# Kernel tuning notes

Hardware: AMD Instinct MI355X
Metric: run time of the kernel (lower is better)

Reference implementation:

```python
import jax, jax.numpy as jnp
import numpy as np

QMAX = 127.0  # int8 symmetric fake-quant (Brevitas weight_bit_width=8)

def fake_quant_w(w):
    # per-tensor symmetric int8 fake quantization of weights
    scale = jnp.maximum(jnp.max(jnp.abs(w)), 1e-8) / QMAX
    return jnp.clip(jnp.round(w / scale), -QMAX, QMAX) * scale

def conv2d(x, w, b=None, padding=0, groups=1):
    y = jax.lax.conv_general_dilated(
        x, w, window_strides=(1, 1),
        padding=[(padding, padding), (padding, padding)],
        feature_group_count=groups,
        dimension_numbers=('NCHW', 'OIHW', 'NCHW'))
    if b is not None:
        y = y + b[None, :, None, None]
    return y

def setup_inputs() -> dict:
    key = jax.random.key(0)
    ks = jax.random.split(key, 12)
    B, H, W = 16, 96, 128
    cor_planes = 4 * (2 * 3 + 1) ** 2  # 196
    def rnd(k, shape, fan_in):
        return jax.random.normal(k, shape, dtype=jnp.float32) * (1.0 / np.sqrt(fan_in))
    return {
        'flow': jax.random.normal(ks[0], (B, 2, H, W), dtype=jnp.float32),
        'corr': jax.random.normal(ks[1], (B, cor_planes, H, W), dtype=jnp.float32),
        'Wc1': rnd(ks[2], (96, cor_planes, 1, 1), cor_planes),
        'bc1': rnd(ks[3], (96,), cor_planes),
        'Wf1': rnd(ks[4], (64, 2, 1, 1), 2),
        'bf1': rnd(ks[5], (64,), 2),
        'Wf2': rnd(ks[6], (32, 64, 1, 1), 64),
        'bf2': rnd(ks[7], (32,), 64),
        'Wd': rnd(ks[8], (128, 1, 3, 3), 9),   # depthwise, groups=128, no bias
        'Wp': rnd(ks[9], (80, 128, 1, 1), 128),
        'bp': rnd(ks[10], (80,), 128),
    }

def reference(flow, corr, Wc1, bc1, Wf1, bf1, Wf2, bf2, Wd, Wp, bp):
    relu = jax.nn.relu
    cor = relu(conv2d(corr, fake_quant_w(Wc1), bc1))              # [B,96,H,W]
    flo = relu(conv2d(flow, fake_quant_w(Wf1), bf1))              # [B,64,H,W]
    flo = relu(conv2d(flo, fake_quant_w(Wf2), bf2))               # [B,32,H,W]
    cor_flo = jnp.concatenate([cor, flo], axis=1)                 # [B,128,H,W]
    dw = conv2d(cor_flo, fake_quant_w(Wd), None, padding=1, groups=128)  # depthwise 3x3
    out = relu(conv2d(dw, fake_quant_w(Wp), bp))                  # [B,80,H,W]
    return jnp.concatenate([out, flow], axis=1)                   # [B,82,H,W]
```

## Files before the change

kernel.cpp:

```cpp
#include <hip/hip_runtime.h>

typedef unsigned short ushort_t;
typedef __attribute__((ext_vector_type(8))) short short8;
typedef __attribute__((ext_vector_type(4))) float f32x4;

#define HWp 12288
#define NB  16

#define OFF_WFRAG1 0
#define OFF_WFRAG2 43008
#define OFF_WF1T   63488
#define OFF_WF2T   64000
#define OFF_WDQ    72192
#define OFF_CORFLO 131072

__device__ __forceinline__ short f2bf(float f) {
  unsigned u = __builtin_bit_cast(unsigned, f);
  u = (u + 0x7FFFu + ((u >> 16) & 1u)) >> 16;
  return (short)u;
}
__device__ __forceinline__ float bf2f(ushort_t u) {
  return __builtin_bit_cast(float, (unsigned)u << 16);
}
__device__ __forceinline__ int swz(int a16) { return a16 ^ ((a16 >> 2) & 3); }

__global__ __launch_bounds__(1024) void quant_pack(
    const float* __restrict__ Wc1, const float* __restrict__ Wf1,
    const float* __restrict__ Wf2, const float* __restrict__ Wd,
    const float* __restrict__ Wp, char* __restrict__ ws)
{
  int t = blockIdx.x;
  const float* src; int n;
  if      (t == 0) { src = Wc1; n = 96*196; }
  else if (t == 1) { src = Wf1; n = 128; }
  else if (t == 2) { src = Wf2; n = 2048; }
  else if (t == 3) { src = Wd;  n = 1152; }
  else             { src = Wp;  n = 10240; }

  __shared__ float red[1024];
  float m = 0.f;
  for (int i = threadIdx.x; i < n; i += 1024) m = fmaxf(m, fabsf(src[i]));
  red[threadIdx.x] = m;
  __syncthreads();
  for (int s = 512; s > 0; s >>= 1) {
    if (threadIdx.x < s) red[threadIdx.x] = fmaxf(red[threadIdx.x], red[threadIdx.x + s]);
    __syncthreads();
  }
  float scale = fmaxf(red[0], 1e-8f) / 127.0f;

  if (t == 0) {
    short* dst = (short*)(ws + OFF_WFRAG1);
    for (int i = threadIdx.x; i < 21504; i += 1024) {
      int j = i & 7, lane = (i >> 3) & 63, rest = i >> 9;
      int mb = rest % 6, kb = rest / 6;
      int ch = mb*16 + (lane & 15);
      int k  = kb*32 + ((lane >> 4) << 3) + j;
      float v = 0.f;
      if (k < 196) {
        float q = rintf(src[ch*196 + k] / scale);
        v = fminf(fmaxf(q, -127.f), 127.f) * scale;
      }
      dst[i] = f2bf(v);
    }
  } else if (t == 4) {
    short* dst = (short*)(ws + OFF_WFRAG2);
    for (int i = threadIdx.x; i < 10240; i += 1024) {
      int j = i & 7, lane = (i >> 3) & 63, rest = i >> 9;
      int mb = rest % 5, kb = rest / 5;
      int ch = mb*16 + (lane & 15);
      int k  = kb*32 + ((lane >> 4) << 3) + j;
      float q = rintf(src[ch*128 + k] / scale);
      dst[i] = f2bf(fminf(fmaxf(q, -127.f), 127.f) * scale);
    }
  } else if (t == 1) {
    float* dst = (float*)(ws + OFF_WF1T);
    for (int i = threadIdx.x; i < 128; i += 1024) {
      int o = i >> 1, c = i & 1;
      float q = rintf(src[i] / scale);
      dst[c*64 + o] = fminf(fmaxf(q, -127.f), 127.f) * scale;
    }
  } else if (t == 2) {
    float* dst = (float*)(ws + OFF_WF2T);
    for (int i = threadIdx.x; i < 2048; i += 1024) {
      int o = i >> 6, c = i & 63;
      float q = rintf(src[i] / scale);
      dst[c*32 + o] = fminf(fmaxf(q, -127.f), 127.f) * scale;
    }
  } else {
    float* dst = (float*)(ws + OFF_WDQ);
    for (int i = threadIdx.x; i < 1152; i += 1024) {
      float q = rintf(src[i] / scale);
      dst[i] = fminf(fmaxf(q, -127.f), 127.f) * scale;
    }
  }
}

__global__ __launch_bounds__(256, 4) void stage1_mfma(
    const float* __restrict__ corr, const float* __restrict__ bc1,
    char* __restrict__ ws)
{
  __shared__ ushort_t s_act[28*64*8];
  const int t = threadIdx.x;
  const int b = blockIdx.x / 192;
  const int pix_base = (blockIdx.x % 192) * 64;

  for (int i = t; i < 1792; i += 256) {
    int px = i & 63, kg = i >> 6, k0 = kg << 3;
    const float* src = corr + ((size_t)b*196 + k0)*HWp + pix_base + px;
    short8 v;
    if (kg < 24) {
#pragma unroll
      for (int j = 0; j < 8; j++) v[j] = f2bf(src[(size_t)j*HWp]);
    } else if (kg == 24) {
#pragma unroll
      for (int j = 0; j < 8; j++) v[j] = (j < 4) ? f2bf(src[(size_t)j*HWp]) : (short)0;
    } else {
#pragma unroll
      for (int j = 0; j < 8; j++) v[j] = 0;
    }
    *(short8*)&s_act[(size_t)i*8] = v;
  }
  __syncthreads();

  const int wave = t >> 6, lane = t & 63;
  const int lg = lane >> 4, lr = lane & 15;
  const int pxl = wave*16 + lr;

  f32x4 acc[6];
#pragma unroll
  for (int i = 0; i < 6; i++) acc[i] = f32x4{0.f, 0.f, 0.f, 0.f};

  const short8* wf = (const short8*)(ws + OFF_WFRAG1);
  for (int kb = 0; kb < 7; kb++) {
    short8 aa = *(const short8*)&s_act[((kb*4 + lg)*64 + pxl)*8];
#pragma unroll
    for (int mb = 0; mb < 6; mb++) {
      short8 w = wf[(kb*6 + mb)*64 + lane];
      acc[mb] = __builtin_amdgcn_mfma_f32_16x16x32_bf16(w, aa, acc[mb], 0, 0, 0);
    }
  }

  ushort_t* cf = (ushort_t*)(ws + OFF_CORFLO) + (size_t)b*128*HWp + pix_base + pxl;
#pragma unroll
  for (int mb = 0; mb < 6; mb++)
#pragma unroll
    for (int r = 0; r < 4; r++) {
      int ch = mb*16 + lg*4 + r;
      float v = fmaxf(acc[mb][r] + bc1[ch], 0.f);
      cf[(size_t)ch * HWp] = (ushort_t)f2bf(v);
    }
}

__global__ __launch_bounds__(256) void flow_path(
    const float* __restrict__ flow, const float* __restrict__ bf1,
    const float* __restrict__ bf2, char* __restrict__ ws)
{
  int pix = blockIdx.x * 256 + threadIdx.x;
  int b = pix / HWp, p = pix - b*HWp;
  const float* wf1t = (const float*)(ws + OFF_WF1T);
  const float* wf2t = (const float*)(ws + OFF_WF2T);
  float x0 = flow[(size_t)(b*2 + 0)*HWp + p];
  float x1 = flow[(size_t)(b*2 + 1)*HWp + p];
  float h[64];
#pragma unroll
  for (int o = 0; o < 64; o++)
    h[o] = fmaxf(bf1[o] + x0*wf1t[o] + x1*wf1t[64 + o], 0.f);
  float g[32];
#pragma unroll
  for (int o = 0; o < 32; o++) g[o] = bf2[o];
#pragma unroll
  for (int c = 0; c < 64; c++) {
    float a = h[c];
#pragma unroll
    for (int o = 0; o < 32; o++) g[o] += a * wf2t[c*32 + o];
  }
  ushort_t* dst = (ushort_t*)(ws + OFF_CORFLO) + ((size_t)b*128 + 96)*HWp + p;
#pragma unroll
  for (int o = 0; o < 32; o++)
    dst[(size_t)o*HWp] = (ushort_t)f2bf(fmaxf(g[o], 0.f));
}

__global__ __launch_bounds__(256, 3) void stage2_mfma(
    const float* __restrict__ bp, const float* __restrict__ flow,
    const char* __restrict__ ws, float* __restrict__ out)
{
  __shared__ ushort_t inb[32*4*128];
  __shared__ ushort_t actc[4*256*8];
  const int t = threadIdx.x;
  const int tile = blockIdx.x;
  const int b = blockIdx.y;
  const int y0 = tile * 2;
  const int wave = t >> 6, lane = t & 63;
  const int lg = lane >> 4, lr = lane & 15;
  const int row = lane >> 5, xq = lane & 31, x0 = xq*4;
  const int y = y0 + row;
  const ushort_t* cf = (const ushort_t*)(ws + OFF_CORFLO) + (size_t)b*128*HWp;
  const float* wdq = (const float*)(ws + OFF_WDQ);
  const short8* wfr2 = (const short8*)(ws + OFF_WFRAG2);

  f32x4 acc[4][5];
#pragma unroll
  for (int g = 0; g < 4; g++)
#pragma unroll
    for (int mb = 0; mb < 5; mb++) acc[g][mb] = f32x4{0.f, 0.f, 0.f, 0.f};

  const bool has_up = (y > 0), has_dn = (y < 95);
  const bool has_l = (x0 > 0), has_r = (x0 < 124);

  for (int cb = 0; cb < 4; cb++) {
    for (int c = t; c < 2048; c += 256) {
      int x16 = c & 15, ry = (c >> 4) & 3, ch = c >> 6;
      int yc = y0 - 1 + ry; yc = yc < 0 ? 0 : (yc > 95 ? 95 : yc);
      const ushort_t* src = cf + (size_t)(cb*32 + ch)*HWp + yc*128 + x16*8;
      *(short8*)&inb[c*8] = *(const short8*)src;
    }
    __syncthreads();

    float vv[4][8];
#pragma unroll
    for (int i = 0; i < 8; i++) {
      int ch = wave*8 + i;
      const float* w = wdq + (size_t)(cb*32 + ch)*9;
      float o0 = 0.f, o1 = 0.f, o2 = 0.f, o3 = 0.f;
      const ushort_t* rp = &inb[(ch*4 + row)*128 + x0];
#pragma unroll
      for (int dy = 0; dy < 3; dy++) {
        if ((dy == 0 && !has_up) || (dy == 2 && !has_dn)) continue;
        const ushort_t* r = rp + dy*128;
        float c0 = bf2f(r[0]), c1 = bf2f(r[1]), c2 = bf2f(r[2]), c3 = bf2f(r[3]);
        float lf = has_l ? bf2f(r[-1]) : 0.f;
        float rt = has_r ? bf2f(r[4]) : 0.f;
        float w0 = w[dy*3], w1 = w[dy*3 + 1], w2 = w[dy*3 + 2];
        o0 += w0*lf + w1*c0 + w2*c1;
        o1 += w0*c0 + w1*c1 + w2*c2;
        o2 += w0*c1 + w1*c2 + w2*c3;
        o3 += w0*c2 + w1*c3 + w2*rt;
      }
      vv[0][i] = o0; vv[1][i] = o1; vv[2][i] = o2; vv[3][i] = o3;
    }
#pragma unroll
    for (int p = 0; p < 4; p++) {
      short8 pk;
#pragma unroll
      for (int i = 0; i < 8; i++) pk[i] = f2bf(vv[p][i]);
      *(short8*)&actc[swz(wave*256 + row*128 + x0 + p)*8] = pk;
    }
    __syncthreads();

    short8 wv[5];
#pragma unroll
    for (int mb = 0; mb < 5; mb++) wv[mb] = wfr2[(cb*5 + mb)*64 + lane];
#pragma unroll
    for (int g = 0; g < 4; g++) {
      int px = wave*64 + g*16 + lr;
      short8 aa = *(const short8*)&actc[swz(lg*256 + px)*8];
#pragma unroll
      for (int mb = 0; mb < 5; mb++)
        acc[g][mb] = __builtin_amdgcn_mfma_f32_16x16x32_bf16(wv[mb], aa, acc[g][mb], 0, 0, 0);
    }
  }

  const size_t pix0 = (size_t)y0 * 128;
#pragma unroll
  for (int g = 0; g < 4; g++) {
    int px = wave*64 + g*16 + lr;
    float* dst = out + ((size_t)b*82)*HWp + pix0 + px;
#pragma unroll
    for (int mb = 0; mb < 5; mb++)
#pragma unroll
      for (int r = 0; r < 4; r++) {
        int ch = mb*16 + lg*4 + r;
        dst[(size_t)ch*HWp] = fmaxf(acc[g][mb][r] + bp[ch], 0.f);
      }
  }
  {
    size_t p = pix0 + t;
    out[((size_t)b*82 + 80)*HWp + p] = flow[((size_t)b*2 + 0)*HWp + p];
    out[((size_t)b*82 + 81)*HWp + p] = flow[((size_t)b*2 + 1)*HWp + p];
  }
}

extern "C" void kernel_launch(void* const* d_in, const int* in_sizes, int n_in,
                              void* d_out, int out_size, void* d_ws, size_t ws_size,
                              hipStream_t stream)
{
  const float* flow = (const float*)d_in[0];
  const float* corr = (const float*)d_in[1];
  const float* Wc1  = (const float*)d_in[2];
  const float* bc1  = (const float*)d_in[3];
  const float* Wf1  = (const float*)d_in[4];
  const float* bf1  = (const float*)d_in[5];
  const float* Wf2  = (const float*)d_in[6];
  const float* bf2  = (const float*)d_in[7];
  const float* Wd   = (const float*)d_in[8];
  const float* Wp   = (const float*)d_in[9];
  const float* bp   = (const float*)d_in[10];
  char* ws = (char*)d_ws;
  float* out = (float*)d_out;

  hipLaunchKernelGGL(quant_pack, dim3(5), dim3(1024), 0, stream,
                     Wc1, Wf1, Wf2, Wd, Wp, ws);
  hipLaunchKernelGGL(stage1_mfma, dim3(3072), dim3(256), 0, stream,
                     corr, bc1, ws);
  hipLaunchKernelGGL(flow_path, dim3(768), dim3(256), 0, stream,
                     flow, bf1, bf2, ws);
  hipLaunchKernelGGL(stage2_mfma, dim3(48, 16), dim3(256), 0, stream,
                     bp, flow, ws, out);
}
```

Before: 360.7 us.

## Load stage1 activations directly into registers and prefetch stage2 tiles via LDS-DMA

```diff
diff --git a/kernel.cpp b/kernel.cpp
--- a/kernel.cpp
+++ b/kernel.cpp
@@ -23,6 +23,12 @@
   return __builtin_bit_cast(float, (unsigned)u << 16);
 }
 __device__ __forceinline__ int swz(int a16) { return a16 ^ ((a16 >> 2) & 3); }
+
+__device__ __forceinline__ void gload_lds16(const void* g, void* l) {
+  __builtin_amdgcn_global_load_lds(
+      (const __attribute__((address_space(1))) unsigned*)g,
+      (__attribute__((address_space(3))) unsigned*)l, 16, 0, 0);
+}
 
 __global__ __launch_bounds__(1024) void quant_pack(
     const float* __restrict__ Wc1, const float* __restrict__ Wf1,
@@ -95,60 +101,58 @@
   }
 }
 
-__global__ __launch_bounds__(256, 4) void stage1_mfma(
+__global__ __launch_bounds__(256, 3) void stage1_mfma(
     const float* __restrict__ corr, const float* __restrict__ bc1,
     char* __restrict__ ws)
 {
-  __shared__ ushort_t s_act[28*64*8];
   const int t = threadIdx.x;
-  const int b = blockIdx.x / 192;
-  const int pix_base = (blockIdx.x % 192) * 64;
-
-  for (int i = t; i < 1792; i += 256) {
-    int px = i & 63, kg = i >> 6, k0 = kg << 3;
-    const float* src = corr + ((size_t)b*196 + k0)*HWp + pix_base + px;
-    short8 v;
-    if (kg < 24) {
-#pragma unroll
-      for (int j = 0; j < 8; j++) v[j] = f2bf(src[(size_t)j*HWp]);
-    } else if (kg == 24) {
-#pragma unroll
-      for (int j = 0; j < 8; j++) v[j] = (j < 4) ? f2bf(src[(size_t)j*HWp]) : (short)0;
-    } else {
-#pragma unroll
-      for (int j = 0; j < 8; j++) v[j] = 0;
-    }
-    *(short8*)&s_act[(size_t)i*8] = v;
-  }
-  __syncthreads();
-
   const int wave = t >> 6, lane = t & 63;
-  const int lg = lane >> 4, lr = lane & 15;
-  const int pxl = wave*16 + lr;
-
-  f32x4 acc[6];
-#pragma unroll
-  for (int i = 0; i < 6; i++) acc[i] = f32x4{0.f, 0.f, 0.f, 0.f};
+  const int lg = (lane >> 4) & 3, lr = lane & 15;
+  const int b = blockIdx.x / 96;
+  const int px0 = (blockIdx.x % 96) * 128 + wave * 32;
+
+  f32x4 acc[2][6];
+#pragma unroll
+  for (int f = 0; f < 2; f++)
+#pragma unroll
+    for (int mb = 0; mb < 6; mb++) acc[f][mb] = f32x4{0.f, 0.f, 0.f, 0.f};
 
   const short8* wf = (const short8*)(ws + OFF_WFRAG1);
+  const float* cbase = corr + (size_t)b * 196 * HWp;
+
+#pragma unroll
   for (int kb = 0; kb < 7; kb++) {
-    short8 aa = *(const short8*)&s_act[((kb*4 + lg)*64 + pxl)*8];
+    short8 aa[2];
+#pragma unroll
+    for (int f = 0; f < 2; f++) {
+      const float* src = cbase + (size_t)(kb*32 + lg*8) * HWp + px0 + f*16 + lr;
+#pragma unroll
+      for (int j = 0; j < 8; j++) {
+        int k = kb*32 + lg*8 + j;
+        float v = (k < 196) ? src[(size_t)j * HWp] : 0.f;
+        aa[f][j] = f2bf(v);
+      }
+    }
 #pragma unroll
     for (int mb = 0; mb < 6; mb++) {
       short8 w = wf[(kb*6 + mb)*64 + lane];
-      acc[mb] = __builtin_amdgcn_mfma_f32_16x16x32_bf16(w, aa, acc[mb], 0, 0, 0);
-    }
-  }
-
-  ushort_t* cf = (ushort_t*)(ws + OFF_CORFLO) + (size_t)b*128*HWp + pix_base + pxl;
-#pragma unroll
-  for (int mb = 0; mb < 6; mb++)
-#pragma unroll
-    for (int r = 0; r < 4; r++) {
-      int ch = mb*16 + lg*4 + r;
-      float v = fmaxf(acc[mb][r] + bc1[ch], 0.f);
-      cf[(size_t)ch * HWp] = (ushort_t)f2bf(v);
-    }
+      acc[0][mb] = __builtin_amdgcn_mfma_f32_16x16x32_bf16(w, aa[0], acc[0][mb], 0, 0, 0);
+      acc[1][mb] = __builtin_amdgcn_mfma_f32_16x16x32_bf16(w, aa[1], acc[1][mb], 0, 0, 0);
+    }
+  }
+
+  ushort_t* cf = (ushort_t*)(ws + OFF_CORFLO) + (size_t)b*128*HWp;
+#pragma unroll
+  for (int f = 0; f < 2; f++) {
+    int px = px0 + f*16 + lr;
+#pragma unroll
+    for (int mb = 0; mb < 6; mb++)
+#pragma unroll
+      for (int r = 0; r < 4; r++) {
+        int ch = mb*16 + lg*4 + r;
+        cf[(size_t)ch*HWp + px] = (ushort_t)f2bf(fmaxf(acc[f][mb][r] + bc1[ch], 0.f));
+      }
+  }
 }
 
 __global__ __launch_bounds__(256) void flow_path(
@@ -207,13 +211,15 @@
   const bool has_up = (y > 0), has_dn = (y < 95);
   const bool has_l = (x0 > 0), has_r = (x0 < 124);
 
+#pragma unroll
+  for (int i = 0; i < 8; i++) {
+    int u = i*256 + t;
+    int x16 = u & 15, ry = (u >> 4) & 3, ch = u >> 6;
+    int yc = y0 - 1 + ry; yc = yc < 0 ? 0 : (yc > 95 ? 95 : yc);
+    gload_lds16(cf + (size_t)ch*HWp + yc*128 + x16*8, &inb[u*8]);
+  }
+
   for (int cb = 0; cb < 4; cb++) {
-    for (int c = t; c < 2048; c += 256) {
-      int x16 = c & 15, ry = (c >> 4) & 3, ch = c >> 6;
-      int yc = y0 - 1 + ry; yc = yc < 0 ? 0 : (yc > 95 ? 95 : yc);
-      const ushort_t* src = cf + (size_t)(cb*32 + ch)*HWp + yc*128 + x16*8;
-      *(short8*)&inb[c*8] = *(const short8*)src;
-    }
     __syncthreads();
 
     float vv[4][8];
@@ -246,6 +252,16 @@
       *(short8*)&actc[swz(wave*256 + row*128 + x0 + p)*8] = pk;
     }
     __syncthreads();
+
+    if (cb < 3) {
+#pragma unroll
+      for (int i = 0; i < 8; i++) {
+        int u = i*256 + t;
+        int x16 = u & 15, ry = (u >> 4) & 3, ch = u >> 6;
+        int yc = y0 - 1 + ry; yc = yc < 0 ? 0 : (yc > 95 ? 95 : yc);
+        gload_lds16(cf + (size_t)((cb+1)*32 + ch)*HWp + yc*128 + x16*8, &inb[u*8]);
+      }
+    }
 
     short8 wv[5];
 #pragma unroll
@@ -300,7 +316,7 @@
 
   hipLaunchKernelGGL(quant_pack, dim3(5), dim3(1024), 0, stream,
                      Wc1, Wf1, Wf2, Wd, Wp, ws);
-  hipLaunchKernelGGL(stage1_mfma, dim3(3072), dim3(256), 0, stream,
+  hipLaunchKernelGGL(stage1_mfma, dim3(1536), dim3(256), 0, stream,
                      corr, bc1, ws);
   hipLaunchKernelGGL(flow_path, dim3(768), dim3(256), 0, stream,
                      flow, bf1, bf2, ws);
```

Result: faster. 351.1 us (-2.6%).
